# Kernel tuning notes

Measured on AMD Instinct MI355X. Metric: run time of the kernel, lower is better.

## Reference

```python
import jax, jax.numpy as jnp
import numpy as np

NUM_EXPERTS = 8
TOP_K = 2


def setup_inputs() -> dict:
    key = jax.random.key(0)
    k1, k2, k3, k4, k5 = jax.random.split(key, 5)
    B, S, H, F, E = 4, 2048, 1024, 4096, NUM_EXPERTS
    return {
        "hidden_states": jax.random.normal(k1, (B, S, H), dtype=jnp.float32),
        "gate_w": jax.random.normal(k2, (E, H), dtype=jnp.float32) * 0.02,
        "w1": jax.random.normal(k3, (E, F, H), dtype=jnp.float32) * 0.02,
        "w3": jax.random.normal(k4, (E, F, H), dtype=jnp.float32) * 0.02,
        "w2": jax.random.normal(k5, (E, H, F), dtype=jnp.float32) * 0.02,
    }


def reference(hidden_states, gate_w, w1, w3, w2):
    B, S, H = hidden_states.shape
    E = gate_w.shape[0]
    x = hidden_states.reshape(-1, H)  # [T, H]
    T = x.shape[0]

    # Router: logits -> fp32 softmax -> top-k -> renormalize (Mixtral)
    router_logits = x @ gate_w.T  # [T, E]
    probs = jax.nn.softmax(router_logits.astype(jnp.float32), axis=-1)
    top_w, top_idx = jax.lax.top_k(probs, TOP_K)  # [T, K]
    top_w = top_w / jnp.sum(top_w, axis=-1, keepdims=True)
    top_w = top_w.astype(x.dtype)

    # Combine weights per (token, expert); zero for unselected experts.
    comb = jnp.zeros((T, E), dtype=x.dtype).at[
        jnp.arange(T)[:, None], top_idx
    ].add(top_w)  # [T, E]

    out = jnp.zeros((T, H), dtype=x.dtype)
    for e in range(E):  # structural loop over distinct expert weights
        h = jax.nn.silu(x @ w1[e].T) * (x @ w3[e].T)  # [T, F]
        out = out + comb[:, e:e + 1] * (h @ w2[e].T)  # [T, H]

    return out.reshape(B, S, H), router_logits
```

## Files before the change

kernel.cpp:

```cpp
#include <hip/hip_runtime.h>
#include <hip/hip_bf16.h>
#include <stdint.h>

#define T_TOK 8192
#define H_DIM 1024
#define F_DIM 4096
#define NEXP  8
#define CAP        17408
#define CAP_TILES  136

typedef __attribute__((ext_vector_type(8))) short bf16x8;
typedef __attribute__((ext_vector_type(4))) float f32x4;

#define AS1 __attribute__((address_space(1)))
#define AS3 __attribute__((address_space(3)))

__device__ __forceinline__ void gload_lds16(const void* g, void* l) {
  __builtin_amdgcn_global_load_lds((const AS1 void*)g, (AS3 void*)l, 16, 0, 0);
}

struct TK { int i0, i1; float w0, w1; };

__global__ __launch_bounds__(256) void router_kernel(
    const float* __restrict__ x, const float* __restrict__ gw,
    float* __restrict__ logits, int* __restrict__ counts, TK* __restrict__ tk)
{
  const int lane = threadIdx.x & 63;
  const int t = blockIdx.x * 4 + (threadIdx.x >> 6);
  const float* xp = x + (size_t)t * H_DIM;
  float xr[16];
#pragma unroll
  for (int i = 0; i < 16; ++i) xr[i] = xp[lane + i * 64];
  float lg[NEXP];
#pragma unroll
  for (int e = 0; e < NEXP; ++e) {
    const float* gp = gw + e * H_DIM;
    float acc = 0.f;
#pragma unroll
    for (int i = 0; i < 16; ++i) acc += xr[i] * gp[lane + i * 64];
#pragma unroll
    for (int s = 32; s > 0; s >>= 1) acc += __shfl_xor(acc, s, 64);
    lg[e] = acc;
  }
  if (lane < NEXP) logits[(size_t)t * NEXP + lane] = lg[lane];
  if (lane == 0) {
    int i0 = 0; float m0 = lg[0];
#pragma unroll
    for (int e = 1; e < NEXP; ++e) if (lg[e] > m0) { m0 = lg[e]; i0 = e; }
    int i1 = -1; float m1 = -1e30f;
#pragma unroll
    for (int e = 0; e < NEXP; ++e) if (e != i0 && lg[e] > m1) { m1 = lg[e]; i1 = e; }
    float r = expf(m1 - m0);
    float w0 = 1.f / (1.f + r);
    float w1 = r / (1.f + r);
    TK v; v.i0 = i0; v.i1 = i1; v.w0 = w0; v.w1 = w1;
    tk[t] = v;
    atomicAdd(&counts[i0], 1);
    atomicAdd(&counts[i1], 1);
  }
}

__global__ __launch_bounds__(256) void scan_kernel(
    const int* __restrict__ counts, int* __restrict__ offs,
    int* __restrict__ cursor, int* __restrict__ tile_expert)
{
  __shared__ int so[NEXP + 1];
  const int tid = threadIdx.x;
  if (tid == 0) {
    int o = 0;
    for (int e = 0; e < NEXP; ++e) {
      so[e] = o; offs[e] = o; cursor[e] = o;
      o += (counts[e] + 127) & ~127;
    }
    so[NEXP] = o; offs[NEXP] = o;
  }
  __syncthreads();
  for (int ti = tid; ti < CAP_TILES; ti += 256) {
    int row = ti * 128;
    int e = NEXP - 1;
#pragma unroll
    for (int k = 0; k < NEXP; ++k)
      if (row >= so[k] && row < so[k + 1]) { e = k; break; }
    tile_expert[ti] = e;
  }
}

__global__ __launch_bounds__(256) void scatter_kernel(
    const TK* __restrict__ tk, int* __restrict__ cursor,
    int* __restrict__ pair_tok, float* __restrict__ pair_w,
    int2* __restrict__ inv)
{
  int t = blockIdx.x * 256 + threadIdx.x;
  if (t >= T_TOK) return;
  TK v = tk[t];
  int p0 = atomicAdd(&cursor[v.i0], 1);
  pair_tok[p0] = t; pair_w[p0] = v.w0;
  int p1 = atomicAdd(&cursor[v.i1], 1);
  pair_tok[p1] = t; pair_w[p1] = v.w1;
  inv[t] = make_int2(p0, p1);
}

union Pack8 { __hip_bfloat16 o[8]; uint4 u; };

__global__ __launch_bounds__(256) void gather_kernel(
    const float* __restrict__ x, const int* __restrict__ pair_tok,
    __hip_bfloat16* __restrict__ xg)
{
  int idx = blockIdx.x * 256 + threadIdx.x;
  int row = idx >> 7;
  int c8  = (idx & 127) << 3;
  int tok = pair_tok[row];
  const float4* src = reinterpret_cast<const float4*>(x + (size_t)tok * H_DIM + c8);
  float4 a = src[0], b = src[1];
  Pack8 pk;
  pk.o[0] = __float2bfloat16(a.x); pk.o[1] = __float2bfloat16(a.y);
  pk.o[2] = __float2bfloat16(a.z); pk.o[3] = __float2bfloat16(a.w);
  pk.o[4] = __float2bfloat16(b.x); pk.o[5] = __float2bfloat16(b.y);
  pk.o[6] = __float2bfloat16(b.z); pk.o[7] = __float2bfloat16(b.w);
  *reinterpret_cast<uint4*>(xg + (size_t)row * H_DIM + c8) = pk.u;
}

__global__ __launch_bounds__(256) void convert_kernel(
    const float* __restrict__ src, __hip_bfloat16* __restrict__ dst, long long n)
{
  long long i = ((long long)blockIdx.x * 256 + threadIdx.x) * 8;
  if (i >= n) return;
  float4 a = *reinterpret_cast<const float4*>(src + i);
  float4 b = *reinterpret_cast<const float4*>(src + i + 4);
  Pack8 pk;
  pk.o[0] = __float2bfloat16(a.x); pk.o[1] = __float2bfloat16(a.y);
  pk.o[2] = __float2bfloat16(a.z); pk.o[3] = __float2bfloat16(a.w);
  pk.o[4] = __float2bfloat16(b.x); pk.o[5] = __float2bfloat16(b.y);
  pk.o[6] = __float2bfloat16(b.z); pk.o[7] = __float2bfloat16(b.w);
  *reinterpret_cast<uint4*>(dst + i) = pk.u;
}


__global__ __launch_bounds__(256, 2) void gemm1_kernel(
    const __hip_bfloat16* __restrict__ xg,
    const __hip_bfloat16* __restrict__ w1b,
    const __hip_bfloat16* __restrict__ w3b,
    const int* __restrict__ tile_expert,
    __hip_bfloat16* __restrict__ h)
{
  __shared__ __hip_bfloat16 sA[128 * 32], sB1[128 * 32], sB3[128 * 32];
  const int n_ = blockIdx.x;
  const int swz = (n_ & 7) * 544 + (n_ >> 3);
  const int tf = swz & 31;
  const int tm = swz >> 5;
  const int e  = tile_expert[tm];
  const int tid = threadIdx.x;

  const __hip_bfloat16* A  = xg  + (size_t)tm * 128 * H_DIM;
  const __hip_bfloat16* B1 = w1b + (size_t)e * F_DIM * H_DIM + (size_t)tf * 128 * H_DIM;
  const __hip_bfloat16* B3 = w3b + (size_t)e * F_DIM * H_DIM + (size_t)tf * 128 * H_DIM;

  const int r     = tid >> 2;
  const int s_src = (tid & 3) ^ ((r >> 1) & 3);
  const int kc    = s_src * 8;
  const int lo    = tid * 8;

  f32x4 acc1[4][4] = {};
  f32x4 acc3[4][4] = {};

  const int wv = tid >> 6, lane = tid & 63;
  const int wr = wv >> 1, wc = wv & 1;
  const int l16 = lane & 15, lk = lane >> 4;
  const int rdk = (lk * 8) ^ (((l16 >> 1) & 3) * 8);

  for (int kt = 0; kt < H_DIM / 32; ++kt) {
    __syncthreads();
    const int gk = kt * 32 + kc;
    gload_lds16(A  + (size_t)r * H_DIM + gk,          &sA [lo]);
    gload_lds16(A  + (size_t)(r + 64) * H_DIM + gk,   &sA [2048 + lo]);
    gload_lds16(B1 + (size_t)r * H_DIM + gk,          &sB1[lo]);
    gload_lds16(B1 + (size_t)(r + 64) * H_DIM + gk,   &sB1[2048 + lo]);
    gload_lds16(B3 + (size_t)r * H_DIM + gk,          &sB3[lo]);
    gload_lds16(B3 + (size_t)(r + 64) * H_DIM + gk,   &sB3[2048 + lo]);
    __syncthreads();

    bf16x8 af[4], b1f[4], b3f[4];
#pragma unroll
    for (int m = 0; m < 4; ++m)
      af[m] = *reinterpret_cast<const bf16x8*>(&sA[(wr * 64 + m * 16 + l16) * 32 + rdk]);
#pragma unroll
    for (int n = 0; n < 4; ++n) {
      b1f[n] = *reinterpret_cast<const bf16x8*>(&sB1[(wc * 64 + n * 16 + l16) * 32 + rdk]);
      b3f[n] = *reinterpret_cast<const bf16x8*>(&sB3[(wc * 64 + n * 16 + l16) * 32 + rdk]);
    }
#pragma unroll
    for (int m = 0; m < 4; ++m)
#pragma unroll
      for (int n = 0; n < 4; ++n) {
        acc1[m][n] = __builtin_amdgcn_mfma_f32_16x16x32_bf16(af[m], b1f[n], acc1[m][n], 0, 0, 0);
        acc3[m][n] = __builtin_amdgcn_mfma_f32_16x16x32_bf16(af[m], b3f[n], acc3[m][n], 0, 0, 0);
      }
  }

  __hip_bfloat16* hp = h + (size_t)tm * 128 * F_DIM + (size_t)tf * 128;
#pragma unroll
  for (int m = 0; m < 4; ++m)
#pragma unroll
    for (int n = 0; n < 4; ++n)
#pragma unroll
      for (int j = 0; j < 4; ++j) {
        int row = wr * 64 + m * 16 + lk * 4 + j;
        int col = wc * 64 + n * 16 + l16;
        float c1 = acc1[m][n][j];
        float c3 = acc3[m][n][j];
        float s  = c1 / (1.f + expf(-c1));
        hp[(size_t)row * F_DIM + col] = __float2bfloat16(s * c3);
      }
}

__global__ __launch_bounds__(256, 2) void gemm2_kernel(
    const __hip_bfloat16* __restrict__ h,
    const __hip_bfloat16* __restrict__ w2b,
    const int* __restrict__ tile_expert,
    const float* __restrict__ pair_w,
    float* __restrict__ y)
{
  __shared__ __hip_bfloat16 sA[128 * 32], sB[128 * 32];
  const int n_ = blockIdx.x;
  const int swz = (n_ & 7) * 136 + (n_ >> 3);
  const int tn = swz & 7;
  const int tm = swz >> 3;
  const int e  = tile_expert[tm];
  const int tid = threadIdx.x;

  const __hip_bfloat16* A = h   + (size_t)tm * 128 * F_DIM;
  const __hip_bfloat16* B = w2b + (size_t)e * H_DIM * F_DIM + (size_t)tn * 128 * F_DIM;

  const int r     = tid >> 2;
  const int s_src = (tid & 3) ^ ((r >> 1) & 3);
  const int kc    = s_src * 8;
  const int lo    = tid * 8;

  f32x4 acc[4][4] = {};
  const int wv = tid >> 6, lane = tid & 63;
  const int wr = wv >> 1, wc = wv & 1;
  const int l16 = lane & 15, lk = lane >> 4;
  const int rdk = (lk * 8) ^ (((l16 >> 1) & 3) * 8);

  for (int kt = 0; kt < F_DIM / 32; ++kt) {
    __syncthreads();
    const int gk = kt * 32 + kc;
    gload_lds16(A + (size_t)r * F_DIM + gk,          &sA[lo]);
    gload_lds16(A + (size_t)(r + 64) * F_DIM + gk,   &sA[2048 + lo]);
    gload_lds16(B + (size_t)r * F_DIM + gk,          &sB[lo]);
    gload_lds16(B + (size_t)(r + 64) * F_DIM + gk,   &sB[2048 + lo]);
    __syncthreads();

    bf16x8 af[4], bf[4];
#pragma unroll
    for (int m = 0; m < 4; ++m)
      af[m] = *reinterpret_cast<const bf16x8*>(&sA[(wr * 64 + m * 16 + l16) * 32 + rdk]);
#pragma unroll
    for (int n = 0; n < 4; ++n)
      bf[n] = *reinterpret_cast<const bf16x8*>(&sB[(wc * 64 + n * 16 + l16) * 32 + rdk]);
#pragma unroll
    for (int m = 0; m < 4; ++m)
#pragma unroll
      for (int n = 0; n < 4; ++n)
        acc[m][n] = __builtin_amdgcn_mfma_f32_16x16x32_bf16(af[m], bf[n], acc[m][n], 0, 0, 0);
  }

#pragma unroll
  for (int m = 0; m < 4; ++m)
#pragma unroll
    for (int j = 0; j < 4; ++j) {
      int rowg = tm * 128 + wr * 64 + m * 16 + lk * 4 + j;
      float w = pair_w[rowg];
      float* op = y + (size_t)rowg * H_DIM + tn * 128 + wc * 64;
#pragma unroll
      for (int n = 0; n < 4; ++n)
        op[n * 16 + l16] = w * acc[m][n][j];
    }
}

__global__ __launch_bounds__(256) void combine_kernel(
    const float* __restrict__ y, const int2* __restrict__ inv,
    float* __restrict__ out)
{
  int idx = blockIdx.x * 256 + threadIdx.x;
  int t  = idx >> 8;
  int c  = (idx & 255) << 2;
  int2 p = inv[t];
  float4 a = *reinterpret_cast<const float4*>(y + (size_t)p.x * H_DIM + c);
  float4 b = *reinterpret_cast<const float4*>(y + (size_t)p.y * H_DIM + c);
  float4 o; o.x = a.x + b.x; o.y = a.y + b.y; o.z = a.z + b.z; o.w = a.w + b.w;
  *reinterpret_cast<float4*>(out + (size_t)t * H_DIM + c) = o;
}

#define WS_COUNTS   0
#define WS_CURSOR   32
#define WS_OFFS     64
#define WS_TILEEXP  128
#define WS_TK       1024
#define WS_PAIRTOK  132096
#define WS_PAIRW    201728
#define WS_ZERO_BYTES 271360
#define WS_INV      271360
#define WS_XG       336896ll
#define WS_W1       (WS_XG + 35651584ll)
#define WS_W3       (WS_W1 + 67108864ll)
#define WS_W2       (WS_W3 + 67108864ll)
#define WS_H        (WS_W2 + 67108864ll)
#define WS_Y        WS_XG

extern "C" void kernel_launch(void* const* d_in, const int* in_sizes, int n_in,
                              void* d_out, int out_size, void* d_ws, size_t ws_size,
                              hipStream_t stream) {
  const float* x  = (const float*)d_in[0];
  const float* gw = (const float*)d_in[1];
  const float* w1 = (const float*)d_in[2];
  const float* w3 = (const float*)d_in[3];
  const float* w2 = (const float*)d_in[4];
  float* out    = (float*)d_out;
  float* logits = out + (size_t)T_TOK * H_DIM;

  char* ws = (char*)d_ws;
  int*   counts   = (int*)(ws + WS_COUNTS);
  int*   cursor   = (int*)(ws + WS_CURSOR);
  int*   offs     = (int*)(ws + WS_OFFS);
  int*   tile_exp = (int*)(ws + WS_TILEEXP);
  TK*    tk       = (TK*)(ws + WS_TK);
  int*   pair_tok = (int*)(ws + WS_PAIRTOK);
  float* pair_w   = (float*)(ws + WS_PAIRW);
  int2*  inv      = (int2*)(ws + WS_INV);
  __hip_bfloat16* xg  = (__hip_bfloat16*)(ws + WS_XG);
  __hip_bfloat16* w1b = (__hip_bfloat16*)(ws + WS_W1);
  __hip_bfloat16* w3b = (__hip_bfloat16*)(ws + WS_W3);
  __hip_bfloat16* w2b = (__hip_bfloat16*)(ws + WS_W2);
  __hip_bfloat16* hbuf = (__hip_bfloat16*)(ws + WS_H);
  float* ybuf = (float*)(ws + WS_Y);

  hipMemsetAsync(d_ws, 0, WS_ZERO_BYTES, stream);

  const long long nW = (long long)NEXP * F_DIM * H_DIM;
  convert_kernel<<<16384, 256, 0, stream>>>(w1, w1b, nW);
  convert_kernel<<<16384, 256, 0, stream>>>(w3, w3b, nW);
  convert_kernel<<<16384, 256, 0, stream>>>(w2, w2b, nW);

  router_kernel<<<T_TOK / 4, 256, 0, stream>>>(x, gw, logits, counts, tk);
  scan_kernel<<<1, 256, 0, stream>>>(counts, offs, cursor, tile_exp);
  scatter_kernel<<<T_TOK / 256, 256, 0, stream>>>(tk, cursor, pair_tok, pair_w, inv);
  gather_kernel<<<(CAP * 128) / 256, 256, 0, stream>>>(x, pair_tok, xg);

  gemm1_kernel<<<CAP_TILES * (F_DIM / 128), 256, 0, stream>>>(
      xg, w1b, w3b, tile_exp, hbuf);
  gemm2_kernel<<<CAP_TILES * (H_DIM / 128), 256, 0, stream>>>(
      hbuf, w2b, tile_exp, pair_w, ybuf);
  combine_kernel<<<(T_TOK * H_DIM / 4) / 256, 256, 0, stream>>>(ybuf, inv, out);
}
```

Baseline: 1.011 ms.

## Retile MoE GEMMs with deeper K-step, narrower gemm1 N, and nontemporal stores

Both expert GEMMs now load a K-slice of 64 per barrier instead of 32, with an 8-way XOR swizzle for the wider LDS rows, so each pair of syncs covers twice the MFMA work. gemm1 narrows its N tile to 64 (halving the accumulators for w1/w3), doubles the grid, and raises launch bounds to 3 blocks per CU. The block-to-tile mapping is changed so consecutive blocks walk token tiles rather than F or H tiles. Intermediate h and y writes use nontemporal stores to avoid polluting cache. Register pressure from 3 blocks per CU and lower A-tile reuse in gemm1 are the trade-offs.

```diff
diff --git a/kernel.cpp b/kernel.cpp
--- a/kernel.cpp
+++ b/kernel.cpp
@@ -7,7 +7,7 @@
 #define F_DIM 4096
 #define NEXP  8
 #define CAP        17408
-#define CAP_TILES  136
+#define CT128      136
 
 typedef __attribute__((ext_vector_type(8))) short bf16x8;
 typedef __attribute__((ext_vector_type(4))) float f32x4;
@@ -17,6 +17,11 @@
 
 __device__ __forceinline__ void gload_lds16(const void* g, void* l) {
   __builtin_amdgcn_global_load_lds((const AS1 void*)g, (AS3 void*)l, 16, 0, 0);
+}
+
+__device__ __forceinline__ void nt_store_bf16(__hip_bfloat16* p, float v) {
+  union { __hip_bfloat16 b; short s; } u; u.b = __float2bfloat16(v);
+  __builtin_nontemporal_store(u.s, (short*)p);
 }
 
 struct TK { int i0, i1; float w0, w1; };
@@ -75,7 +80,7 @@
     so[NEXP] = o; offs[NEXP] = o;
   }
   __syncthreads();
-  for (int ti = tid; ti < CAP_TILES; ti += 256) {
+  for (int ti = tid; ti < CT128; ti += 256) {
     int row = ti * 128;
     int e = NEXP - 1;
 #pragma unroll
@@ -136,145 +141,157 @@
 }
 
 
-__global__ __launch_bounds__(256, 2) void gemm1_kernel(
+__global__ __launch_bounds__(256, 3) void gemm1_kernel(
     const __hip_bfloat16* __restrict__ xg,
     const __hip_bfloat16* __restrict__ w1b,
     const __hip_bfloat16* __restrict__ w3b,
     const int* __restrict__ tile_expert,
     __hip_bfloat16* __restrict__ h)
 {
-  __shared__ __hip_bfloat16 sA[128 * 32], sB1[128 * 32], sB3[128 * 32];
-  const int n_ = blockIdx.x;
-  const int swz = (n_ & 7) * 544 + (n_ >> 3);
-  const int tf = swz & 31;
-  const int tm = swz >> 5;
-  const int e  = tile_expert[tm];
+  __shared__ __hip_bfloat16 sA[128 * 64], sB1[64 * 64], sB3[64 * 64];
+  const int n_  = blockIdx.x;
+  const int idx = (n_ & 7) * 1088 + (n_ >> 3);
+  const int tm  = idx % 136;
+  const int tf  = idx / 136;
+  const int e   = tile_expert[tm];
   const int tid = threadIdx.x;
 
   const __hip_bfloat16* A  = xg  + (size_t)tm * 128 * H_DIM;
-  const __hip_bfloat16* B1 = w1b + (size_t)e * F_DIM * H_DIM + (size_t)tf * 128 * H_DIM;
-  const __hip_bfloat16* B3 = w3b + (size_t)e * F_DIM * H_DIM + (size_t)tf * 128 * H_DIM;
-
-  const int r     = tid >> 2;
-  const int s_src = (tid & 3) ^ ((r >> 1) & 3);
-  const int kc    = s_src * 8;
-  const int lo    = tid * 8;
-
-  f32x4 acc1[4][4] = {};
-  f32x4 acc3[4][4] = {};
+  const __hip_bfloat16* B1 = w1b + (size_t)e * F_DIM * H_DIM + (size_t)tf * 64 * H_DIM;
+  const __hip_bfloat16* B3 = w3b + (size_t)e * F_DIM * H_DIM + (size_t)tf * 64 * H_DIM;
+
+  const int rs  = tid >> 3;
+  const int sl  = tid & 7;
+  const int xsl = (sl ^ (rs & 7)) * 8;
+  const int dst = rs * 64 + sl * 8;
 
   const int wv = tid >> 6, lane = tid & 63;
-  const int wr = wv >> 1, wc = wv & 1;
+  const int wm = wv >> 1, wn = wv & 1;
   const int l16 = lane & 15, lk = lane >> 4;
-  const int rdk = (lk * 8) ^ (((l16 >> 1) & 3) * 8);
-
-  for (int kt = 0; kt < H_DIM / 32; ++kt) {
+  const int ps0 = ((0 + lk) ^ (l16 & 7)) * 8;
+  const int ps1 = ((4 + lk) ^ (l16 & 7)) * 8;
+
+  f32x4 acc1[4][2] = {};
+  f32x4 acc3[4][2] = {};
+
+  for (int kt = 0; kt < H_DIM / 64; ++kt) {
     __syncthreads();
-    const int gk = kt * 32 + kc;
-    gload_lds16(A  + (size_t)r * H_DIM + gk,          &sA [lo]);
-    gload_lds16(A  + (size_t)(r + 64) * H_DIM + gk,   &sA [2048 + lo]);
-    gload_lds16(B1 + (size_t)r * H_DIM + gk,          &sB1[lo]);
-    gload_lds16(B1 + (size_t)(r + 64) * H_DIM + gk,   &sB1[2048 + lo]);
-    gload_lds16(B3 + (size_t)r * H_DIM + gk,          &sB3[lo]);
-    gload_lds16(B3 + (size_t)(r + 64) * H_DIM + gk,   &sB3[2048 + lo]);
+    const int gk = kt * 64 + xsl;
+#pragma unroll
+    for (int c = 0; c < 4; ++c)
+      gload_lds16(A + (size_t)(rs + 32 * c) * H_DIM + gk, &sA[c * 2048 + dst]);
+#pragma unroll
+    for (int c = 0; c < 2; ++c) {
+      gload_lds16(B1 + (size_t)(rs + 32 * c) * H_DIM + gk, &sB1[c * 2048 + dst]);
+      gload_lds16(B3 + (size_t)(rs + 32 * c) * H_DIM + gk, &sB3[c * 2048 + dst]);
+    }
     __syncthreads();
-
-    bf16x8 af[4], b1f[4], b3f[4];
-#pragma unroll
-    for (int m = 0; m < 4; ++m)
-      af[m] = *reinterpret_cast<const bf16x8*>(&sA[(wr * 64 + m * 16 + l16) * 32 + rdk]);
-#pragma unroll
-    for (int n = 0; n < 4; ++n) {
-      b1f[n] = *reinterpret_cast<const bf16x8*>(&sB1[(wc * 64 + n * 16 + l16) * 32 + rdk]);
-      b3f[n] = *reinterpret_cast<const bf16x8*>(&sB3[(wc * 64 + n * 16 + l16) * 32 + rdk]);
-    }
-#pragma unroll
-    for (int m = 0; m < 4; ++m)
-#pragma unroll
-      for (int n = 0; n < 4; ++n) {
-        acc1[m][n] = __builtin_amdgcn_mfma_f32_16x16x32_bf16(af[m], b1f[n], acc1[m][n], 0, 0, 0);
-        acc3[m][n] = __builtin_amdgcn_mfma_f32_16x16x32_bf16(af[m], b3f[n], acc3[m][n], 0, 0, 0);
+#pragma unroll
+    for (int ks = 0; ks < 2; ++ks) {
+      const int ps = ks ? ps1 : ps0;
+      bf16x8 a[4], b1[2], b3[2];
+#pragma unroll
+      for (int m = 0; m < 4; ++m)
+        a[m] = *reinterpret_cast<const bf16x8*>(&sA[(wm * 64 + m * 16 + l16) * 64 + ps]);
+#pragma unroll
+      for (int nf = 0; nf < 2; ++nf) {
+        b1[nf] = *reinterpret_cast<const bf16x8*>(&sB1[(wn * 32 + nf * 16 + l16) * 64 + ps]);
+        b3[nf] = *reinterpret_cast<const bf16x8*>(&sB3[(wn * 32 + nf * 16 + l16) * 64 + ps]);
       }
-  }
-
-  __hip_bfloat16* hp = h + (size_t)tm * 128 * F_DIM + (size_t)tf * 128;
+#pragma unroll
+      for (int m = 0; m < 4; ++m)
+#pragma unroll
+        for (int nf = 0; nf < 2; ++nf) {
+          acc1[m][nf] = __builtin_amdgcn_mfma_f32_16x16x32_bf16(a[m], b1[nf], acc1[m][nf], 0, 0, 0);
+          acc3[m][nf] = __builtin_amdgcn_mfma_f32_16x16x32_bf16(a[m], b3[nf], acc3[m][nf], 0, 0, 0);
+        }
+    }
+  }
+
+  __hip_bfloat16* hp = h + (size_t)tm * 128 * F_DIM + (size_t)tf * 64;
 #pragma unroll
   for (int m = 0; m < 4; ++m)
 #pragma unroll
-    for (int n = 0; n < 4; ++n)
+    for (int nf = 0; nf < 2; ++nf)
 #pragma unroll
       for (int j = 0; j < 4; ++j) {
-        int row = wr * 64 + m * 16 + lk * 4 + j;
-        int col = wc * 64 + n * 16 + l16;
-        float c1 = acc1[m][n][j];
-        float c3 = acc3[m][n][j];
+        int row = wm * 64 + m * 16 + lk * 4 + j;
+        int col = wn * 32 + nf * 16 + l16;
+        float c1 = acc1[m][nf][j];
+        float c3 = acc3[m][nf][j];
         float s  = c1 / (1.f + expf(-c1));
-        hp[(size_t)row * F_DIM + col] = __float2bfloat16(s * c3);
+        nt_store_bf16(&hp[(size_t)row * F_DIM + col], s * c3);
       }
 }
 
-__global__ __launch_bounds__(256, 2) void gemm2_kernel(
+__global__ __launch_bounds__(256, 3) void gemm2_kernel(
     const __hip_bfloat16* __restrict__ h,
     const __hip_bfloat16* __restrict__ w2b,
     const int* __restrict__ tile_expert,
     const float* __restrict__ pair_w,
     float* __restrict__ y)
 {
-  __shared__ __hip_bfloat16 sA[128 * 32], sB[128 * 32];
-  const int n_ = blockIdx.x;
-  const int swz = (n_ & 7) * 136 + (n_ >> 3);
-  const int tn = swz & 7;
-  const int tm = swz >> 3;
-  const int e  = tile_expert[tm];
+  __shared__ __hip_bfloat16 sA[128 * 64], sB[128 * 64];
+  const int n_  = blockIdx.x;
+  const int idx = (n_ & 7) * 136 + (n_ >> 3);
+  const int tm  = idx % 136;
+  const int tn  = idx / 136;
+  const int e   = tile_expert[tm];
   const int tid = threadIdx.x;
 
   const __hip_bfloat16* A = h   + (size_t)tm * 128 * F_DIM;
   const __hip_bfloat16* B = w2b + (size_t)e * H_DIM * F_DIM + (size_t)tn * 128 * F_DIM;
 
-  const int r     = tid >> 2;
-  const int s_src = (tid & 3) ^ ((r >> 1) & 3);
-  const int kc    = s_src * 8;
-  const int lo    = tid * 8;
+  const int rs  = tid >> 3;
+  const int sl  = tid & 7;
+  const int xsl = (sl ^ (rs & 7)) * 8;
+  const int dst = rs * 64 + sl * 8;
+
+  const int wv = tid >> 6, lane = tid & 63;
+  const int wm = wv >> 1, wn = wv & 1;
+  const int l16 = lane & 15, lk = lane >> 4;
+  const int ps0 = ((0 + lk) ^ (l16 & 7)) * 8;
+  const int ps1 = ((4 + lk) ^ (l16 & 7)) * 8;
 
   f32x4 acc[4][4] = {};
-  const int wv = tid >> 6, lane = tid & 63;
-  const int wr = wv >> 1, wc = wv & 1;
-  const int l16 = lane & 15, lk = lane >> 4;
-  const int rdk = (lk * 8) ^ (((l16 >> 1) & 3) * 8);
-
-  for (int kt = 0; kt < F_DIM / 32; ++kt) {
+
+  for (int kt = 0; kt < F_DIM / 64; ++kt) {
     __syncthreads();
-    const int gk = kt * 32 + kc;
-    gload_lds16(A + (size_t)r * F_DIM + gk,          &sA[lo]);
-    gload_lds16(A + (size_t)(r + 64) * F_DIM + gk,   &sA[2048 + lo]);
-    gload_lds16(B + (size_t)r * F_DIM + gk,          &sB[lo]);
-    gload_lds16(B + (size_t)(r + 64) * F_DIM + gk,   &sB[2048 + lo]);
+    const int gk = kt * 64 + xsl;
+#pragma unroll
+    for (int c = 0; c < 4; ++c) {
+      gload_lds16(A + (size_t)(rs + 32 * c) * F_DIM + gk, &sA[c * 2048 + dst]);
+      gload_lds16(B + (size_t)(rs + 32 * c) * F_DIM + gk, &sB[c * 2048 + dst]);
+    }
     __syncthreads();
-
-    bf16x8 af[4], bf[4];
-#pragma unroll
-    for (int m = 0; m < 4; ++m)
-      af[m] = *reinterpret_cast<const bf16x8*>(&sA[(wr * 64 + m * 16 + l16) * 32 + rdk]);
-#pragma unroll
-    for (int n = 0; n < 4; ++n)
-      bf[n] = *reinterpret_cast<const bf16x8*>(&sB[(wc * 64 + n * 16 + l16) * 32 + rdk]);
-#pragma unroll
-    for (int m = 0; m < 4; ++m)
-#pragma unroll
-      for (int n = 0; n < 4; ++n)
-        acc[m][n] = __builtin_amdgcn_mfma_f32_16x16x32_bf16(af[m], bf[n], acc[m][n], 0, 0, 0);
+#pragma unroll
+    for (int ks = 0; ks < 2; ++ks) {
+      const int ps = ks ? ps1 : ps0;
+      bf16x8 a[4], b[4];
+#pragma unroll
+      for (int m = 0; m < 4; ++m)
+        a[m] = *reinterpret_cast<const bf16x8*>(&sA[(wm * 64 + m * 16 + l16) * 64 + ps]);
+#pragma unroll
+      for (int nf = 0; nf < 4; ++nf)
+        b[nf] = *reinterpret_cast<const bf16x8*>(&sB[(wn * 64 + nf * 16 + l16) * 64 + ps]);
+#pragma unroll
+      for (int m = 0; m < 4; ++m)
+#pragma unroll
+        for (int nf = 0; nf < 4; ++nf)
+          acc[m][nf] = __builtin_amdgcn_mfma_f32_16x16x32_bf16(a[m], b[nf], acc[m][nf], 0, 0, 0);
+    }
   }
 
 #pragma unroll
   for (int m = 0; m < 4; ++m)
 #pragma unroll
     for (int j = 0; j < 4; ++j) {
-      int rowg = tm * 128 + wr * 64 + m * 16 + lk * 4 + j;
+      int rowg = tm * 128 + wm * 64 + m * 16 + lk * 4 + j;
       float w = pair_w[rowg];
-      float* op = y + (size_t)rowg * H_DIM + tn * 128 + wc * 64;
-#pragma unroll
-      for (int n = 0; n < 4; ++n)
-        op[n * 16 + l16] = w * acc[m][n][j];
+      float* op = y + (size_t)rowg * H_DIM + tn * 128 + wn * 64;
+#pragma unroll
+      for (int nf = 0; nf < 4; ++nf)
+        __builtin_nontemporal_store(w * acc[m][nf][j], op + nf * 16 + l16);
     }
 }
 
@@ -347,9 +364,9 @@
   scatter_kernel<<<T_TOK / 256, 256, 0, stream>>>(tk, cursor, pair_tok, pair_w, inv);
   gather_kernel<<<(CAP * 128) / 256, 256, 0, stream>>>(x, pair_tok, xg);
 
-  gemm1_kernel<<<CAP_TILES * (F_DIM / 128), 256, 0, stream>>>(
+  gemm1_kernel<<<CT128 * (F_DIM / 64), 256, 0, stream>>>(
       xg, w1b, w3b, tile_exp, hbuf);
-  gemm2_kernel<<<CAP_TILES * (H_DIM / 128), 256, 0, stream>>>(
+  gemm2_kernel<<<CT128 * (H_DIM / 128), 256, 0, stream>>>(
       hbuf, w2b, tile_exp, pair_w, ybuf);
   combine_kernel<<<(T_TOK * H_DIM / 4) / 256, 256, 0, stream>>>(ybuf, inv, out);
 }
```

New measurement: 974.6 us. -3.6%, faster.
